# Kernel tuning notes

Hardware: AMD Instinct MI355X
Metric: run time of the kernel (lower is better)

The kernel has to match this reference:

```python
import jax, jax.numpy as jnp
import numpy as np

B, L, D, H = 4, 2048, 1024, 16
DH = D // H
THETA = 100000.0


def setup_inputs() -> dict:
    key = jax.random.key(0)
    k1, k2, k3 = jax.random.split(key, 3)
    std_w = (2.0 / (D + 3 * D)) ** 0.5
    std_o = (2.0 / (D + D)) ** 0.5
    return {
        "x": jax.random.normal(k1, (B, L, D), dtype=jnp.float32),
        "W": jax.random.normal(k2, (3 * D, D), dtype=jnp.float32) * std_w,
        "Wo": jax.random.normal(k3, (D, D), dtype=jnp.float32) * std_o,
    }


def _rope(t):
    # t: [B, H, L, DH]; interleaved pair rotation as in the torch module
    pos = jnp.arange(L, dtype=jnp.float32)
    inv_freq = 1.0 / THETA ** (jnp.arange(0, DH, 2, dtype=jnp.float32) / DH)
    ang = pos[:, None] * inv_freq[None, :]            # [L, DH/2]
    cos = jnp.cos(ang)[:, :, None]                    # [L, DH/2, 1]
    sin = jnp.sin(ang)[:, :, None]
    tp = t.reshape(*t.shape[:-1], DH // 2, 2)         # pairs (x1, x2)
    x1, x2 = tp[..., 0], tp[..., 1]
    rot = jnp.stack([-x2, x1], axis=-1)               # [-x2, x1]
    out = tp * cos + rot * sin
    return out.reshape(*t.shape)


def reference(x, W, Wo):
    # fused QKV projection: weight layout is (t h d) along output dim
    qkv = jnp.einsum('bld,ed->ble', x, W)             # [B, L, 3D]
    qkv = qkv.reshape(B, L, 3, H, DH)
    qkv = jnp.transpose(qkv, (0, 3, 1, 2, 4))         # [B, H, L, 3, DH]
    Q, K, V = qkv[..., 0, :], qkv[..., 1, :], qkv[..., 2, :]
    Q, K = _rope(Q), _rope(K)
    scores = jnp.einsum('bhqd,bhkd->bhqk', Q, K) / (DH ** 0.5)
    causal = jnp.tril(jnp.ones((L, L), dtype=bool))
    scores = jnp.where(causal, scores, -jnp.inf)
    attn = jax.nn.softmax(scores, axis=-1)
    out = jnp.einsum('bhqk,bhkd->bhqd', attn, V)      # [B, H, L, DH]
    out = jnp.transpose(out, (0, 2, 1, 3)).reshape(B, L, D)
    return jnp.einsum('bld,ed->ble', out, Wo)
```

## Files before the change

kernel.cpp:

```cpp
#include <hip/hip_runtime.h>
#include <cstddef>
#include <cstdint>


typedef unsigned short u16;
typedef short bf16x8 __attribute__((ext_vector_type(8)));
typedef float f32x4 __attribute__((ext_vector_type(4)));

#define B_   4
#define L_   2048
#define H_   16
#define DH_  64
#define D_   1024
#define E3_  3072

__device__ __forceinline__ u16 f2bf(float f) {
  unsigned int u = __float_as_uint(f);
  u += 0x7fffu + ((u >> 16) & 1u);
  return (u16)(u >> 16);
}
__device__ __forceinline__ float bf2f(u16 h) {
  return __uint_as_float(((unsigned int)h) << 16);
}
__device__ __forceinline__ unsigned pk2(float a, float b) {
  return ((__float_as_uint(a) + 0x8000u) >> 16) |
         ((__float_as_uint(b) + 0x8000u) & 0xffff0000u);
}
__device__ __forceinline__ float fexp2(float x) {
#if __has_builtin(__builtin_amdgcn_exp2f)
  return __builtin_amdgcn_exp2f(x);
#else
  return exp2f(x);
#endif
}

__device__ __forceinline__ void gload_lds16(const void* g, void* l) {
  auto gp = reinterpret_cast<const uint32_t __attribute__((address_space(1)))*>(
      reinterpret_cast<uintptr_t>(g));
  auto lp = reinterpret_cast<uint32_t __attribute__((address_space(3)))*>(
      reinterpret_cast<uintptr_t>(l));
  __builtin_amdgcn_global_load_lds(gp, lp, 16, 0, 0);
}

__global__ __launch_bounds__(256) void cvt_all(const float* __restrict__ x,
                                               const float* __restrict__ W,
                                               const float* __restrict__ Wo,
                                               u16* __restrict__ xb,
                                               u16* __restrict__ Wb,
                                               u16* __restrict__ Wob) {
  int i = blockIdx.x * 256 + threadIdx.x;
  const float* in;
  u16* out;
  int off;
  if (i < 1048576) {
    in = x; out = xb; off = i;
  } else if (i < 1441792) {
    in = W; out = Wb; off = i - 1048576;
  } else {
    in = Wo; out = Wob; off = i - 1441792;
  }
  const float4* p = (const float4*)in;
  float4 a = p[2 * off], b = p[2 * off + 1];
  uint4 o;
  o.x = (unsigned)f2bf(a.x) | ((unsigned)f2bf(a.y) << 16);
  o.y = (unsigned)f2bf(a.z) | ((unsigned)f2bf(a.w) << 16);
  o.z = (unsigned)f2bf(b.x) | ((unsigned)f2bf(b.y) << 16);
  o.w = (unsigned)f2bf(b.z) | ((unsigned)f2bf(b.w) << 16);
  ((uint4*)out)[off] = o;
}

template <bool OUT_BF16>
__global__ __launch_bounds__(256) void gemm_bt(const u16* __restrict__ A,
                                               const u16* __restrict__ Bm,
                                               void* __restrict__ C, int N, int K) {
  __shared__ __align__(16) u16 As[128 * 64];
  __shared__ __align__(16) u16 Bs[128 * 64];
  const int tid = threadIdx.x;
  const int lane = tid & 63, wave = tid >> 6;
  const int quad = lane >> 4, l15 = lane & 15;
  const int wm = (wave >> 1) << 6, wn = (wave & 1) << 6;
  const int m0 = blockIdx.y << 7, n0 = blockIdx.x << 7;

  f32x4 acc[4][4];
#pragma unroll
  for (int i = 0; i < 4; ++i)
#pragma unroll
    for (int j = 0; j < 4; ++j) acc[i][j] = {0.f, 0.f, 0.f, 0.f};

  const int sr = lane >> 3;
  const int sg = (lane & 7) ^ sr;

  for (int k0 = 0; k0 < K; k0 += 64) {
#pragma unroll
    for (int it = 0; it < 4; ++it) {
      const int chunk = wave + it * 4;
      const int row = chunk * 8 + sr;
      gload_lds16(A + (size_t)(m0 + row) * K + k0 + sg * 8, As + chunk * 512);
      gload_lds16(Bm + (size_t)(n0 + row) * K + k0 + sg * 8, Bs + chunk * 512);
    }
    __syncthreads();
#pragma unroll
    for (int ks = 0; ks < 2; ++ks) {
      bf16x8 af[4], bfr[4];
#pragma unroll
      for (int i = 0; i < 4; ++i)
        af[i] = *(const bf16x8*)(As + (wm + i * 16 + l15) * 64 +
                                 (((ks * 4 + quad) ^ (l15 & 7)) * 8));
#pragma unroll
      for (int j = 0; j < 4; ++j)
        bfr[j] = *(const bf16x8*)(Bs + (wn + j * 16 + l15) * 64 +
                                  (((ks * 4 + quad) ^ (l15 & 7)) * 8));
#pragma unroll
      for (int i = 0; i < 4; ++i)
#pragma unroll
        for (int j = 0; j < 4; ++j)
          acc[i][j] = __builtin_amdgcn_mfma_f32_16x16x32_bf16(af[i], bfr[j],
                                                              acc[i][j],
                                                              0, 0, 0);
    }
    __syncthreads();
  }
#pragma unroll
  for (int i = 0; i < 4; ++i) {
    int row = m0 + wm + i * 16 + quad * 4;
#pragma unroll
    for (int j = 0; j < 4; ++j) {
      int col = n0 + wn + j * 16 + l15;
#pragma unroll
      for (int r = 0; r < 4; ++r) {
        if (OUT_BF16)
          ((u16*)C)[(size_t)(row + r) * N + col] = f2bf(acc[i][j][r]);
        else
          ((float*)C)[(size_t)(row + r) * N + col] = acc[i][j][r];
      }
    }
  }
}

__global__ __launch_bounds__(256) void prep(u16* __restrict__ qkvb,
                                            u16* __restrict__ Vt) {
  __shared__ uint32_t tile[64 * 36];
  const int bid = blockIdx.x;
  const int tid = threadIdx.x;
  if (bid < 4096) {
    const int bl = bid * 2 + (tid >> 7);
    const int l = bl & (L_ - 1);
    const int t7 = tid & 127;
    const int c = t7 & 7, h = t7 >> 3;
    u16* p = qkvb + (size_t)bl * E3_ + D_ + h * DH_ + c * 8;
    uint4 v = *(const uint4*)p;
    unsigned* w = (unsigned*)&v;
#pragma unroll
    for (int j = 0; j < 4; ++j) {
      const int d2 = c * 4 + j;
      float inv = exp2f((float)d2 * -0.5190512648261504f);
      float ang = (float)l * inv;
      float sn = __sinf(ang), cs = __cosf(ang);
      float x1 = bf2f((u16)(w[j] & 0xffffu)), x2 = bf2f((u16)(w[j] >> 16));
      w[j] = (unsigned)f2bf(x1 * cs - x2 * sn) |
             ((unsigned)f2bf(x2 * cs + x1 * sn) << 16);
    }
    *(uint4*)p = v;
  } else {
    const int q = bid - 4096;
    const int bh = q >> 5, b = bh >> 4, h = bh & 15;
    const int lbase = (q & 31) << 6;
    {
      const int ur = tid >> 3, c = tid & 7;
      const u16* src = qkvb + (size_t)(b * L_ + lbase + 2 * ur) * E3_ +
                       2 * D_ + h * DH_ + c * 8;
      uint4 va = *(const uint4*)src;
      uint4 vb = *(const uint4*)(src + E3_);
      const unsigned* pa = (const unsigned*)&va;
      const unsigned* pb = (const unsigned*)&vb;
      const int us = ur ^ (c << 2);
#pragma unroll
      for (int qq = 0; qq < 4; ++qq) {
        const int d0 = c * 8 + 2 * qq;
        tile[d0 * 36 + us] = (pa[qq] & 0xffffu) | (pb[qq] << 16);
        tile[(d0 + 1) * 36 + us] = (pa[qq] >> 16) | (pb[qq] & 0xffff0000u);
      }
    }
    __syncthreads();
    const uint4* t4 = (const uint4*)tile;
#pragma unroll
    for (int it = 0; it < 2; ++it) {
      const int u = it * 256 + tid;
      const int d = u >> 3, lc = u & 7;
      uint4 v = t4[d * 9 + (lc ^ (d >> 3))];
      *(uint4*)(Vt + (size_t)(bh * DH_ + d) * L_ + lbase + lc * 8) = v;
    }
  }
}

__global__ __launch_bounds__(512) void attn(const u16* __restrict__ qkvb,
                                            const u16* __restrict__ Vt,
                                            u16* __restrict__ Ob) {
  __shared__ __align__(16) u16 Ks[2][64 * 64];
  __shared__ __align__(16) u16 Vs[2][64 * 64];
  __shared__ __align__(16) u16 Ps[8][16 * 72];
  const int bh = blockIdx.y, b = bh >> 4, h = bh & 15;
  const int pair = blockIdx.x;
  const int tid = threadIdx.x;
  const int lane = tid & 63, wave = tid >> 6, quad = lane >> 4, l15 = lane & 15;
  u16* pw = Ps[wave];

  const int srow = wave * 8 + (lane >> 3);
  const int sgran = (lane & 7) ^ (lane >> 3);
  const u16* ksrc0 =
      qkvb + (size_t)(b * L_ + srow) * E3_ + D_ + h * DH_ + sgran * 8;
  const u16* vsrc0 = Vt + (size_t)(bh * DH_ + srow) * L_ + sgran * 8;
  const int ldst = wave * 512;

  bf16x8 ones;
#pragma unroll
  for (int i = 0; i < 8; ++i) ones[i] = (short)0x3F80;

  for (int a = 0; a < 2; ++a) {
    const int qbase = (a ? pair : (15 - pair)) << 7;
    const int rb = qbase + wave * 16;
    const int qg = rb + l15;

    bf16x8 qf[2];
    {
      const u16* qp = qkvb + (size_t)(b * L_ + qg) * E3_ + h * DH_;
      bf16x8 raw0 = *(const bf16x8*)(qp + quad * 8);
      bf16x8 raw1 = *(const bf16x8*)(qp + 32 + quad * 8);
      const float qsc = 0.18033688011112042f;
#pragma unroll
      for (int f = 0; f < 2; ++f) {
        bf16x8 raw = f ? raw1 : raw0;
        bf16x8 o;
#pragma unroll
        for (int j = 0; j < 4; ++j) {
          const int d2 = f * 16 + quad * 4 + j;
          float inv = exp2f((float)d2 * -0.5190512648261504f);
          float ang = (float)qg * inv;
          float sn = __sinf(ang), cs = __cosf(ang);
          float x1 = bf2f((u16)raw[2 * j]), x2 = bf2f((u16)raw[2 * j + 1]);
          o[2 * j] = (short)f2bf((x1 * cs - x2 * sn) * qsc);
          o[2 * j + 1] = (short)f2bf((x2 * cs + x1 * sn) * qsc);
        }
        qf[f] = o;
      }
    }

    f32x4 acc[4], lacc;
    lacc = {0.f, 0.f, 0.f, 0.f};
#pragma unroll
    for (int j = 0; j < 4; ++j) acc[j] = {0.f, 0.f, 0.f, 0.f};

    gload_lds16(ksrc0, Ks[0] + ldst);
    gload_lds16(vsrc0, Vs[0] + ldst);
    __syncthreads();

    const int kend = qbase + 128;
    int cur = 0;
    for (int kb = 0; kb < kend; kb += 64, cur ^= 1) {
      if (kb + 64 < kend) {
        gload_lds16(ksrc0 + (size_t)(kb + 64) * E3_, Ks[cur ^ 1] + ldst);
        gload_lds16(vsrc0 + (kb + 64), Vs[cur ^ 1] + ldst);
      }
      const u16* kcur = Ks[cur];
      const u16* vcur = Vs[cur];

      f32x4 st[4];
#pragma unroll
      for (int t = 0; t < 4; ++t) st[t] = {0.f, 0.f, 0.f, 0.f};
      __builtin_amdgcn_s_setprio(1);
#pragma unroll
      for (int ks = 0; ks < 2; ++ks) {
        bf16x8 kf[4];
#pragma unroll
        for (int t = 0; t < 4; ++t)
          kf[t] = *(const bf16x8*)(kcur + (t * 16 + l15) * 64 +
                                   (((ks * 4 + quad) ^ (l15 & 7)) * 8));
#pragma unroll
        for (int t = 0; t < 4; ++t)
          st[t] = __builtin_amdgcn_mfma_f32_16x16x32_bf16(kf[t], qf[ks],
                                                          st[t], 0, 0, 0);
      }
      __builtin_amdgcn_s_setprio(0);

      {
        const bool dg = (kb + 63 > rb);
#pragma unroll
        for (int t = 0; t < 4; ++t) {
          const int kg0 = kb + t * 16 + quad * 4;
          float p0, p1, p2, p3;
          if (dg) {
            p0 = (kg0 + 0 > qg) ? 0.f : fexp2(st[t][0]);
            p1 = (kg0 + 1 > qg) ? 0.f : fexp2(st[t][1]);
            p2 = (kg0 + 2 > qg) ? 0.f : fexp2(st[t][2]);
            p3 = (kg0 + 3 > qg) ? 0.f : fexp2(st[t][3]);
          } else {
            p0 = fexp2(st[t][0]);
            p1 = fexp2(st[t][1]);
            p2 = fexp2(st[t][2]);
            p3 = fexp2(st[t][3]);
          }
          uint2 pkd = {pk2(p0, p1), pk2(p2, p3)};
          *(uint2*)(pw + l15 * 72 + t * 16 + quad * 4) = pkd;
        }
      }
      asm volatile("s_waitcnt lgkmcnt(0)" ::: "memory");
      __builtin_amdgcn_sched_barrier(0);

      __builtin_amdgcn_s_setprio(1);
#pragma unroll
      for (int ks = 0; ks < 2; ++ks) {
        bf16x8 vf[4];
#pragma unroll
        for (int j = 0; j < 4; ++j)
          vf[j] = *(const bf16x8*)(vcur + (j * 16 + l15) * 64 +
                                   (((ks * 4 + quad) ^ (l15 & 7)) * 8));
        bf16x8 pf = *(const bf16x8*)(pw + l15 * 72 + ks * 32 + quad * 8);
        lacc = __builtin_amdgcn_mfma_f32_16x16x32_bf16(ones, pf, lacc,
                                                       0, 0, 0);
#pragma unroll
        for (int j = 0; j < 4; ++j)
          acc[j] = __builtin_amdgcn_mfma_f32_16x16x32_bf16(vf[j], pf,
                                                           acc[j], 0, 0, 0);
      }
      __builtin_amdgcn_s_setprio(0);

      __syncthreads();
    }

    {
      const float rl = 1.0f / lacc[0];
#pragma unroll
      for (int j = 0; j < 4; ++j) {
        uint2 od = {pk2(acc[j][0] * rl, acc[j][1] * rl),
                    pk2(acc[j][2] * rl, acc[j][3] * rl)};
        *(uint2*)(pw + l15 * 72 + j * 16 + quad * 4) = od;
      }
    }
    __syncthreads();
#pragma unroll
    for (int it = 0; it < 2; ++it) {
      int unit = it * 512 + tid;
      int row = unit >> 3, ch = (unit & 7) * 8;
      *(uint4*)(Ob + (size_t)(b * L_ + qbase + row) * D_ + h * DH_ + ch) =
          *(const uint4*)(Ps[row >> 4] + (row & 15) * 72 + ch);
    }
    __syncthreads();
  }
}

extern "C" void kernel_launch(void* const* d_in, const int* in_sizes, int n_in,
                              void* d_out, int out_size, void* d_ws, size_t ws_size,
                              hipStream_t stream) {
  const float* x  = (const float*)d_in[0];
  const float* W  = (const float*)d_in[1];
  const float* Wo = (const float*)d_in[2];
  float* out = (float*)d_out;

  char* ws = (char*)d_ws;
  u16* xb   = (u16*)(ws);
  u16* Wb   = (u16*)(ws + 16777216);
  u16* Wob  = (u16*)(ws + 23068672);
  u16* qkvb = (u16*)(ws + 25165824);
  u16* Vt   = (u16*)(ws + 75497472);
  u16* Ob   = (u16*)(ws + 92274688);

  cvt_all<<<6144, 256, 0, stream>>>(x, W, Wo, xb, Wb, Wob);

  gemm_bt<true><<<dim3(E3_ / 128, (B_ * L_) / 128), 256, 0, stream>>>(
      xb, Wb, qkvb, E3_, D_);

  prep<<<4096 + 2048, 256, 0, stream>>>(qkvb, Vt);

  attn<<<dim3(8, B_ * H_), 512, 0, stream>>>(qkvb, Vt, Ob);

  gemm_bt<false><<<dim3(D_ / 128, (B_ * L_) / 128), 256, 0, stream>>>(
      Ob, Wob, out, D_, D_);
}
```

Measured before the change: 240.7 us.

## Double-buffer LDS tiles in bf16 GEMM to overlap global loads with MFMA

The GEMM kernel now allocates two LDS buffers for A and B tiles, preloads the first k-tile, and prefetches the next k-tile into the alternate buffer while MFMAs consume the current one. This is meant to hide global-to-LDS load latency behind compute instead of stalling at a barrier each iteration. It doubles LDS usage to 64KB per block, which can reduce the number of resident blocks per CU, and relies on the remaining barrier for correctness of buffer reuse.

```diff
diff --git a/kernel.cpp b/kernel.cpp
--- a/kernel.cpp
+++ b/kernel.cpp
@@ -73,8 +73,8 @@
 __global__ __launch_bounds__(256) void gemm_bt(const u16* __restrict__ A,
                                                const u16* __restrict__ Bm,
                                                void* __restrict__ C, int N, int K) {
-  __shared__ __align__(16) u16 As[128 * 64];
-  __shared__ __align__(16) u16 Bs[128 * 64];
+  __shared__ __align__(16) u16 As[2][128 * 64];
+  __shared__ __align__(16) u16 Bs[2][128 * 64];
   const int tid = threadIdx.x;
   const int lane = tid & 63, wave = tid >> 6;
   const int quad = lane >> 4, l15 = lane & 15;
@@ -90,25 +90,41 @@
   const int sr = lane >> 3;
   const int sg = (lane & 7) ^ sr;
 
-  for (int k0 = 0; k0 < K; k0 += 64) {
-#pragma unroll
-    for (int it = 0; it < 4; ++it) {
-      const int chunk = wave + it * 4;
-      const int row = chunk * 8 + sr;
-      gload_lds16(A + (size_t)(m0 + row) * K + k0 + sg * 8, As + chunk * 512);
-      gload_lds16(Bm + (size_t)(n0 + row) * K + k0 + sg * 8, Bs + chunk * 512);
-    }
-    __syncthreads();
+  const u16* asrc = A + (size_t)(m0 + sr) * K + sg * 8;
+  const u16* bsrc = Bm + (size_t)(n0 + sr) * K + sg * 8;
+
+#pragma unroll
+  for (int it = 0; it < 4; ++it) {
+    const int chunk = wave + it * 4;
+    gload_lds16(asrc + (size_t)(chunk * 8) * K, As[0] + chunk * 512);
+    gload_lds16(bsrc + (size_t)(chunk * 8) * K, Bs[0] + chunk * 512);
+  }
+  __syncthreads();
+
+  int cur = 0;
+  for (int k0 = 0; k0 < K; k0 += 64, cur ^= 1) {
+    if (k0 + 64 < K) {
+#pragma unroll
+      for (int it = 0; it < 4; ++it) {
+        const int chunk = wave + it * 4;
+        gload_lds16(asrc + (size_t)(chunk * 8) * K + k0 + 64,
+                    As[cur ^ 1] + chunk * 512);
+        gload_lds16(bsrc + (size_t)(chunk * 8) * K + k0 + 64,
+                    Bs[cur ^ 1] + chunk * 512);
+      }
+    }
+    const u16* as = As[cur];
+    const u16* bs = Bs[cur];
 #pragma unroll
     for (int ks = 0; ks < 2; ++ks) {
       bf16x8 af[4], bfr[4];
 #pragma unroll
       for (int i = 0; i < 4; ++i)
-        af[i] = *(const bf16x8*)(As + (wm + i * 16 + l15) * 64 +
+        af[i] = *(const bf16x8*)(as + (wm + i * 16 + l15) * 64 +
                                  (((ks * 4 + quad) ^ (l15 & 7)) * 8));
 #pragma unroll
       for (int j = 0; j < 4; ++j)
-        bfr[j] = *(const bf16x8*)(Bs + (wn + j * 16 + l15) * 64 +
+        bfr[j] = *(const bf16x8*)(bs + (wn + j * 16 + l15) * 64 +
                                   (((ks * 4 + quad) ^ (l15 & 7)) * 8));
 #pragma unroll
       for (int i = 0; i < 4; ++i)
```

Measured after the change: 241.6 us. About the same (+0.4%).
